# Optimization experiments

Measured on AMD Instinct MI355X. Metric: run time of the kernel, lower is better.

## Reference

```python
import jax, jax.numpy as jnp
import numpy as np
from functools import partial

EPS = 1e-5
TAU = 0.1

def bn(x, g, b, axes):
    m = jnp.mean(x, axis=axes, keepdims=True)
    v = jnp.var(x, axis=axes, keepdims=True)
    return (x - m) * jax.lax.rsqrt(v + EPS) * g + b

def conv(x, w, b):
    # x: NCHW, w: OIHW, stride 1, padding 1
    y = jax.lax.conv_general_dilated(x, w, (1, 1), ((1, 1), (1, 1)),
                                     dimension_numbers=('NCHW', 'OIHW', 'NCHW'))
    return y + b[None, :, None, None]

def maxpool2(x):
    return jax.lax.reduce_window(x, -jnp.inf, jax.lax.max, (1, 1, 2, 2), (1, 1, 2, 2), 'VALID')

def setup_inputs() -> dict:
    key = jax.random.key(0)
    ks = jax.random.split(key, 24)
    s = 0.02
    B = 4096
    d = {}
    d['input_data'] = jax.random.normal(ks[0], (B, 3, 32, 32), jnp.float32)
    d['conv1_w'] = jax.random.normal(ks[1], (32, 3, 3, 3), jnp.float32) * s
    d['conv1_b'] = jnp.zeros((32,), jnp.float32)
    d['bn1_g'] = jnp.ones((32,), jnp.float32); d['bn1_b'] = jnp.zeros((32,), jnp.float32)
    d['conv2_w'] = jax.random.normal(ks[2], (64, 32, 3, 3), jnp.float32) * s
    d['conv2_b'] = jnp.zeros((64,), jnp.float32)
    d['bn2_g'] = jnp.ones((64,), jnp.float32); d['bn2_b'] = jnp.zeros((64,), jnp.float32)
    d['conv3_w'] = jax.random.normal(ks[3], (128, 64, 3, 3), jnp.float32) * s
    d['conv3_b'] = jnp.zeros((128,), jnp.float32)
    d['bn3_g'] = jnp.ones((128,), jnp.float32); d['bn3_b'] = jnp.zeros((128,), jnp.float32)
    d['pre_w'] = jax.random.normal(ks[4], (1024, 8192), jnp.float32) * s
    d['pre_b'] = jnp.zeros((1024,), jnp.float32)
    d['bnp_g'] = jnp.ones((1024,), jnp.float32); d['bnp_b'] = jnp.zeros((1024,), jnp.float32)
    d['disc_w'] = jax.random.normal(ks[5], (384, 1024), jnp.float32) * s
    d['disc_b'] = jnp.zeros((384,), jnp.float32)
    d['bnd_g'] = jnp.ones((384,), jnp.float32); d['bnd_b'] = jnp.zeros((384,), jnp.float32)
    d['dfc_w'] = jax.random.normal(ks[6], (2, 384), jnp.float32) * s
    d['dfc_b'] = jnp.zeros((2,), jnp.float32)
    d['sw_w'] = jax.random.normal(ks[7], (2, 384), jnp.float32) * s
    d['sw_b'] = jnp.zeros((2,), jnp.float32)
    # partitioned classifier: P=2, Linear(1024 -> 192) + ReLU + Linear(192 -> 10)
    d['p1_w'] = jax.random.normal(ks[8], (2, 192, 1024), jnp.float32) * s
    d['p1_b'] = jnp.zeros((2, 192), jnp.float32)
    d['p2_w'] = jax.random.normal(ks[9], (2, 10, 192), jnp.float32) * s
    d['p2_b'] = jnp.zeros((2, 10), jnp.float32)
    return d

def reference(input_data, conv1_w, conv1_b, bn1_g, bn1_b, conv2_w, conv2_b, bn2_g, bn2_b,
              conv3_w, conv3_b, bn3_g, bn3_b, pre_w, pre_b, bnp_g, bnp_b,
              disc_w, disc_b, bnd_g, bnd_b, dfc_w, dfc_b, sw_w, sw_b,
              p1_w, p1_b, p2_w, p2_b):
    B = input_data.shape[0]
    # feature extractor
    x = jax.nn.relu(bn(conv(input_data, conv1_w, conv1_b), bn1_g[None, :, None, None], bn1_b[None, :, None, None], (0, 2, 3)))
    x = maxpool2(x)
    x = jax.nn.relu(bn(conv(x, conv2_w, conv2_b), bn2_g[None, :, None, None], bn2_b[None, :, None, None], (0, 2, 3)))
    x = maxpool2(x)
    x = jax.nn.relu(bn(conv(x, conv3_w, conv3_b), bn3_g[None, :, None, None], bn3_b[None, :, None, None], (0, 2, 3)))
    feat = x.reshape(B, -1)  # [B, 8192]
    feat = jax.nn.relu(bn(feat @ pre_w.T + pre_b, bnp_g[None, :], bnp_b[None, :], (0,)))  # [B, 1024]
    # discriminator branch
    dpen = jax.nn.relu(bn(feat @ disc_w.T + disc_b, bnd_g[None, :], bnd_b[None, :], (0,)))  # [B, 384]
    domain_output = dpen @ dfc_w.T + dfc_b  # [B, 2]
    sw_logits = dpen @ sw_w.T + sw_b  # [B, P]
    # gumbel-softmax (soft) + multinomial sample of partition
    key = jax.random.key(42)
    k1, k2 = jax.random.split(key)
    u = jax.random.uniform(k1, sw_logits.shape, jnp.float32, 1e-10, 1.0)
    gumbel = -jnp.log(-jnp.log(u))
    y = jax.nn.softmax((sw_logits + gumbel) / TAU, axis=-1)  # [B, P]
    partition_idx = jax.random.categorical(k2, jnp.log(y + 1e-20), axis=-1)  # [B]
    # per-partition expert MLP computed densely (P=2), then gather chosen partition
    h = jax.nn.relu(jnp.einsum('bi,poi->pbo', feat, p1_w) + p1_b[:, None, :])  # [P, B, 192]
    logits = jnp.einsum('pbo,pco->pbc', h, p2_w) + p2_b[:, None, :]  # [P, B, 10]
    sel = logits[partition_idx, jnp.arange(B)]  # [B, 10]
    # original multiplies single-element stack by full gumbel vector and sums -> scale by sum(y)=1
    class_output_partitioned = sel * jnp.sum(y, axis=1, keepdims=True)
    return (class_output_partitioned, domain_output, partition_idx)
```

## Files before the change

kernel.cpp:

```cpp
#include <hip/hip_runtime.h>
#include <cstdint>
#include <cstddef>

typedef __attribute__((ext_vector_type(8))) short short8;
typedef __attribute__((ext_vector_type(4))) float f32x4;

__host__ __device__ inline void threefry2x32(uint32_t k0, uint32_t k1,
                                             uint32_t x0, uint32_t x1,
                                             uint32_t& o0, uint32_t& o1) {
  uint32_t ks2 = k0 ^ k1 ^ 0x1BD11BDAu;
  uint32_t v0 = x0 + k0, v1 = x1 + k1;
#define TF_R(r) { v0 += v1; v1 = (v1 << (r)) | (v1 >> (32 - (r))); v1 ^= v0; }
  TF_R(13) TF_R(15) TF_R(26) TF_R(6)
  v0 += k1; v1 += ks2 + 1u;
  TF_R(17) TF_R(29) TF_R(16) TF_R(24)
  v0 += ks2; v1 += k0 + 2u;
  TF_R(13) TF_R(15) TF_R(26) TF_R(6)
  v0 += k0; v1 += k1 + 3u;
  TF_R(17) TF_R(29) TF_R(16) TF_R(24)
  v0 += k1; v1 += ks2 + 4u;
  TF_R(13) TF_R(15) TF_R(26) TF_R(6)
  v0 += ks2; v1 += k0 + 5u;
#undef TF_R
  o0 = v0; o1 = v1;
}

__device__ __forceinline__ uint32_t tf_bits32(uint32_t k0, uint32_t k1, uint32_t j) {
  uint32_t o0, o1;
  threefry2x32(k0, k1, 0u, j, o0, o1);
  return o0 ^ o1;
}

__device__ __forceinline__ float u01_from_bits(uint32_t bits) {
  return __uint_as_float((bits >> 9) | 0x3f800000u) - 1.0f;
}

__device__ __forceinline__ float waveSum(float v) {
#pragma unroll
  for (int off = 32; off > 0; off >>= 1) v += __shfl_down(v, off, 64);
  return v;
}

__global__ __launch_bounds__(256) void conv1_fused_kernel(
    const float* __restrict__ in, const float* __restrict__ w,
    float* __restrict__ outraw, float* __restrict__ partials) {
  __shared__ float ins[3 * 34 * 34];
  __shared__ float red[4][64];
  const int b = blockIdx.x, t = threadIdx.x;
  for (int i = t; i < 3 * 34 * 34; i += 256) {
    int ci = i / 1156, r = i % 1156, iy = r / 34, ix = r % 34;
    int y = iy - 1, x = ix - 1;
    float v = 0.f;
    if ((unsigned)y < 32u && (unsigned)x < 32u)
      v = in[(((size_t)b * 3 + ci) * 32 + y) * 32 + x];
    ins[i] = v;
  }
  __syncthreads();
  const int py = t >> 4, px = t & 15, wv = t >> 6, ln = t & 63;
  float win[3][4][4];
#pragma unroll
  for (int ci = 0; ci < 3; ci++)
#pragma unroll
    for (int r = 0; r < 4; r++)
#pragma unroll
      for (int c = 0; c < 4; c++)
        win[ci][r][c] = ins[ci * 1156 + (2 * py + r) * 34 + (2 * px + c)];
#pragma unroll 1
  for (int co = 0; co < 32; co++) {
    float acc00 = 0.f, acc01 = 0.f, acc10 = 0.f, acc11 = 0.f;
#pragma unroll
    for (int ci = 0; ci < 3; ci++) {
      const float* wp = w + (co * 3 + ci) * 9;
#pragma unroll
      for (int dy = 0; dy < 3; dy++)
#pragma unroll
        for (int dx = 0; dx < 3; dx++) {
          float wvv = wp[dy * 3 + dx];
          acc00 += win[ci][dy][dx] * wvv;
          acc01 += win[ci][dy][dx + 1] * wvv;
          acc10 += win[ci][dy + 1][dx] * wvv;
          acc11 += win[ci][dy + 1][dx + 1] * wvv;
        }
    }
    float sm = acc00 + acc01 + acc10 + acc11;
    float sq = acc00 * acc00 + acc01 * acc01 + acc10 * acc10 + acc11 * acc11;
    float s = waveSum(sm), q = waveSum(sq);
    if (ln == 0) { red[wv][2 * co] = s; red[wv][2 * co + 1] = q; }
    float m = fmaxf(fmaxf(acc00, acc01), fmaxf(acc10, acc11));
    outraw[(((size_t)b * 32 + co) * 16 + py) * 16 + px] = m;
  }
  __syncthreads();
  for (int i = t; i < 64; i += 256)
    partials[(size_t)b * 64 + i] = red[0][i] + red[1][i] + red[2][i] + red[3][i];
}

__device__ __forceinline__ uint32_t pack_bf16q(float x) {
  uint32_t u = __float_as_uint(x);
  uint32_t hi = u & 0xffff0000u;
  float r = x - __uint_as_float(hi);
  uint32_t lo = __float_as_uint(r) >> 16;
  return hi | lo;
}

__device__ __forceinline__ uint4 pk4bn(float4 v, float sc, float sh) {
  uint4 o;
  o.x = pack_bf16q(fmaxf(v.x * sc + sh, 0.f));
  o.y = pack_bf16q(fmaxf(v.y * sc + sh, 0.f));
  o.z = pack_bf16q(fmaxf(v.z * sc + sh, 0.f));
  o.w = pack_bf16q(fmaxf(v.w * sc + sh, 0.f));
  return o;
}

__global__ void cvt_bf16q_kernel(const float* X, uint32_t* Y, int n4) {
  int i = blockIdx.x * blockDim.x + threadIdx.x;
  if (i >= n4) return;
  float4 x = ((const float4*)X)[i];
  uint4 o;
  o.x = pack_bf16q(x.x); o.y = pack_bf16q(x.y);
  o.z = pack_bf16q(x.z); o.w = pack_bf16q(x.w);
  ((uint4*)Y)[i] = o;
}

__global__ void prep_w2_kernel(const float* __restrict__ w, short* __restrict__ wh,
                               short* __restrict__ wl) {
  int idx = blockIdx.x * 256 + threadIdx.x;
  if (idx >= 64 * 32 * 9) return;
  int tp = idx % 9, rem = idx / 9;
  int ci = rem % 32, co = rem / 32;
  uint32_t pq = pack_bf16q(w[idx]);
  size_t o = ((size_t)tp * 64 + co) * 32 + ci;
  wh[o] = (short)(pq >> 16);
  wl[o] = (short)(pq & 0xffffu);
}

__global__ void prep_w3_kernel(const float* __restrict__ w, short* __restrict__ wh,
                               short* __restrict__ wl) {
  int idx = blockIdx.x * 256 + threadIdx.x;
  if (idx >= 128 * 64 * 9) return;
  int tp = idx % 9, rem = idx / 9;
  int ci = rem % 64, co = rem / 64;
  uint32_t pq = pack_bf16q(w[idx]);
  size_t o = ((size_t)tp * 128 + co) * 64 + ci;
  wh[o] = (short)(pq >> 16);
  wl[o] = (short)(pq & 0xffffu);
}

#define STORE2(ARR_H, ARR_L, ROW, KB, SW, U, V)                                 \
  {                                                                             \
    uint32_t h0 = (U.x >> 16) | (U.y & 0xffff0000u);                            \
    uint32_t h1 = (U.z >> 16) | (U.w & 0xffff0000u);                            \
    uint32_t h2 = (V.x >> 16) | (V.y & 0xffff0000u);                            \
    uint32_t h3 = (V.z >> 16) | (V.w & 0xffff0000u);                            \
    uint32_t l0 = (U.x & 0xffffu) | (U.y << 16);                                \
    uint32_t l1 = (U.z & 0xffffu) | (U.w << 16);                                \
    uint32_t l2 = (V.x & 0xffffu) | (V.y << 16);                                \
    uint32_t l3 = (V.z & 0xffffu) | (V.w << 16);                                \
    int idx = (ROW) * 32 + ((KB) ^ (SW));                                       \
    *(uint4*)&ARR_H[idx] = make_uint4(h0, h1, h2, h3);                          \
    *(uint4*)&ARR_L[idx] = make_uint4(l0, l1, l2, l3);                          \
  }

__global__ __launch_bounds__(256) void conv2_mfma_kernel(
    const float* __restrict__ in, const float* __restrict__ scale1,
    const float* __restrict__ shift1, const short* __restrict__ wh,
    const short* __restrict__ wl, float* __restrict__ outpool,
    float* __restrict__ partials) {
  __shared__ short Xh[324 * 32], Xl[324 * 32];
  __shared__ float red[4][128];
  const int b = blockIdx.x, t = threadIdx.x;
  for (int i = t; i < 324 * 16; i += 256) {
    int row = i >> 4;
    int py = row / 18, pxx = row % 18;
    if (py == 0 || py == 17 || pxx == 0 || pxx == 17) {
      ((uint32_t*)Xh)[i] = 0u;
      ((uint32_t*)Xl)[i] = 0u;
    }
  }
  for (int i = t; i < 4096; i += 256) {
    int p = i >> 8, px = i & 255;
    int y = px >> 4, x = px & 15;
    float va = in[((size_t)b * 32 + 2 * p) * 256 + px];
    float vb = in[((size_t)b * 32 + 2 * p + 1) * 256 + px];
    va = fmaxf(va * scale1[2 * p] + shift1[2 * p], 0.f);
    vb = fmaxf(vb * scale1[2 * p + 1] + shift1[2 * p + 1], 0.f);
    uint32_t ua = pack_bf16q(va), ub = pack_bf16q(vb);
    uint32_t h = (ua >> 16) | (ub & 0xffff0000u);
    uint32_t l = (ua & 0xffffu) | (ub << 16);
    int row = (y + 1) * 18 + (x + 1);
    int ci2 = (2 * p) ^ ((row & 3) << 3);
    ((uint32_t*)Xh)[(row * 32 + ci2) >> 1] = h;
    ((uint32_t*)Xl)[(row * 32 + ci2) >> 1] = l;
  }
  __syncthreads();
  const int w = t >> 6, l = t & 63;
  const int lr = l & 15, lg = l >> 4;
  f32x4 acc[4][4];
#pragma unroll
  for (int i = 0; i < 4; i++)
#pragma unroll
    for (int j = 0; j < 4; j++) acc[i][j] = (f32x4){0.f, 0.f, 0.f, 0.f};
#pragma unroll 1
  for (int tap = 0; tap < 9; tap++) {
    const int dy = tap / 3, dx = tap % 3;
    short8 awh[4], awl[4];
#pragma unroll
    for (int i = 0; i < 4; i++) {
      size_t off = ((size_t)tap * 64 + i * 16 + lr) * 32 + lg * 8;
      awh[i] = *(const short8*)(wh + off);
      awl[i] = *(const short8*)(wl + off);
    }
    short8 bxh[4], bxl[4];
#pragma unroll
    for (int j = 0; j < 4; j++) {
      int y = w * 4 + j, x = lr;
      int row = (y + dy) * 18 + (x + dx);
      int ci = (lg * 8) ^ ((row & 3) << 3);
      bxh[j] = *(const short8*)&Xh[row * 32 + ci];
      bxl[j] = *(const short8*)&Xl[row * 32 + ci];
    }
#pragma unroll
    for (int i = 0; i < 4; i++)
#pragma unroll
      for (int j = 0; j < 4; j++) {
        acc[i][j] = __builtin_amdgcn_mfma_f32_16x16x32_bf16(awh[i], bxh[j], acc[i][j], 0, 0, 0);
        acc[i][j] = __builtin_amdgcn_mfma_f32_16x16x32_bf16(awh[i], bxl[j], acc[i][j], 0, 0, 0);
        acc[i][j] = __builtin_amdgcn_mfma_f32_16x16x32_bf16(awl[i], bxh[j], acc[i][j], 0, 0, 0);
      }
  }
#pragma unroll
  for (int i = 0; i < 4; i++)
#pragma unroll
    for (int r = 0; r < 4; r++) {
      int co = i * 16 + lg * 4 + r;
      float v0 = acc[i][0][r], v1 = acc[i][1][r], v2 = acc[i][2][r], v3 = acc[i][3][r];
      float s = v0 + v1 + v2 + v3;
      float q = v0 * v0 + v1 * v1 + v2 * v2 + v3 * v3;
#pragma unroll
      for (int off = 1; off <= 8; off <<= 1) {
        s += __shfl_xor(s, off, 64);
        q += __shfl_xor(q, off, 64);
      }
      if (lr == 0) { red[w][2 * co] = s; red[w][2 * co + 1] = q; }
      float h0 = fmaxf(v0, __shfl_xor(v0, 1, 64));
      float h1 = fmaxf(v1, __shfl_xor(v1, 1, 64));
      float h2 = fmaxf(v2, __shfl_xor(v2, 1, 64));
      float h3 = fmaxf(v3, __shfl_xor(v3, 1, 64));
      float pm0 = fmaxf(h0, h1);
      float pm1 = fmaxf(h2, h3);
      if ((lr & 1) == 0) {
        size_t base = ((size_t)b * 64 + co) * 64 + (w * 2) * 8 + (lr >> 1);
        outpool[base] = pm0;
        outpool[base + 8] = pm1;
      }
    }
  __syncthreads();
  for (int i = t; i < 128; i += 256)
    partials[(size_t)b * 128 + i] = red[0][i] + red[1][i] + red[2][i] + red[3][i];
}

__global__ __launch_bounds__(256) void conv3_mfma_kernel(
    const float* __restrict__ in, const float* __restrict__ scale2,
    const float* __restrict__ shift2, const short* __restrict__ wh,
    const short* __restrict__ wl, float* __restrict__ outraw,
    float* __restrict__ partials) {
  __shared__ short Xh[100 * 64], Xl[100 * 64];
  __shared__ float red[256];
  const int b = blockIdx.x, t = threadIdx.x;
  for (int i = t; i < 100 * 32; i += 256) {
    int row = i >> 5;
    int py = row / 10, pxx = row % 10;
    if (py == 0 || py == 9 || pxx == 0 || pxx == 9) {
      ((uint32_t*)Xh)[i] = 0u;
      ((uint32_t*)Xl)[i] = 0u;
    }
  }
  for (int i = t; i < 2048; i += 256) {
    int p = i >> 6, px = i & 63;
    int y = px >> 3, x = px & 7;
    float va = in[((size_t)b * 64 + 2 * p) * 64 + px];
    float vb = in[((size_t)b * 64 + 2 * p + 1) * 64 + px];
    va = fmaxf(va * scale2[2 * p] + shift2[2 * p], 0.f);
    vb = fmaxf(vb * scale2[2 * p + 1] + shift2[2 * p + 1], 0.f);
    uint32_t ua = pack_bf16q(va), ub = pack_bf16q(vb);
    uint32_t h = (ua >> 16) | (ub & 0xffff0000u);
    uint32_t l = (ua & 0xffffu) | (ub << 16);
    int row = (y + 1) * 10 + (x + 1);
    int ci2 = (2 * p) ^ ((row & 7) << 3);
    ((uint32_t*)Xh)[(row * 64 + ci2) >> 1] = h;
    ((uint32_t*)Xl)[(row * 64 + ci2) >> 1] = l;
  }
  __syncthreads();
  const int w = t >> 6, l = t & 63;
  const int lr = l & 15, lg = l >> 4;
  const int co_base = w * 32;
  f32x4 acc[2][4];
#pragma unroll
  for (int i = 0; i < 2; i++)
#pragma unroll
    for (int j = 0; j < 4; j++) acc[i][j] = (f32x4){0.f, 0.f, 0.f, 0.f};
#pragma unroll 1
  for (int tap = 0; tap < 9; tap++) {
    const int dy = tap / 3, dx = tap % 3;
#pragma unroll
    for (int sl = 0; sl < 2; sl++) {
      short8 awh[2], awl[2];
#pragma unroll
      for (int i = 0; i < 2; i++) {
        size_t off = ((size_t)tap * 128 + co_base + i * 16 + lr) * 64 + sl * 32 + lg * 8;
        awh[i] = *(const short8*)(wh + off);
        awl[i] = *(const short8*)(wl + off);
      }
      short8 bxh[4], bxl[4];
#pragma unroll
      for (int j = 0; j < 4; j++) {
        int px = j * 16 + lr;
        int row = ((px >> 3) + dy) * 10 + (px & 7) + dx;
        int ci = (sl * 32 + lg * 8) ^ ((row & 7) << 3);
        bxh[j] = *(const short8*)&Xh[row * 64 + ci];
        bxl[j] = *(const short8*)&Xl[row * 64 + ci];
      }
#pragma unroll
      for (int i = 0; i < 2; i++)
#pragma unroll
        for (int j = 0; j < 4; j++) {
          acc[i][j] = __builtin_amdgcn_mfma_f32_16x16x32_bf16(awh[i], bxh[j], acc[i][j], 0, 0, 0);
          acc[i][j] = __builtin_amdgcn_mfma_f32_16x16x32_bf16(awh[i], bxl[j], acc[i][j], 0, 0, 0);
          acc[i][j] = __builtin_amdgcn_mfma_f32_16x16x32_bf16(awl[i], bxh[j], acc[i][j], 0, 0, 0);
        }
    }
  }
#pragma unroll
  for (int i = 0; i < 2; i++)
#pragma unroll
    for (int r = 0; r < 4; r++) {
      int co = co_base + i * 16 + lg * 4 + r;
      float s = 0.f, q = 0.f;
#pragma unroll
      for (int j = 0; j < 4; j++) {
        float v = acc[i][j][r];
        outraw[((size_t)b * 128 + co) * 64 + j * 16 + lr] = v;
        s += v; q += v * v;
      }
#pragma unroll
      for (int off = 1; off <= 8; off <<= 1) {
        s += __shfl_xor(s, off, 64);
        q += __shfl_xor(q, off, 64);
      }
      if (lr == 0) { red[2 * co] = s; red[2 * co + 1] = q; }
    }
  __syncthreads();
  for (int i = t; i < 256; i += 256) partials[(size_t)b * 256 + i] = red[i];
}

__global__ __launch_bounds__(256) void reduce_partials_kernel(
    const float* __restrict__ partials, int nblk, int Q, double* __restrict__ sums) {
  int q = blockIdx.x;
  double acc = 0.0;
  for (int i = threadIdx.x; i < nblk; i += 256) acc += (double)partials[(size_t)i * Q + q];
  __shared__ double red[256];
  red[threadIdx.x] = acc;
  __syncthreads();
  for (int s = 128; s > 0; s >>= 1) {
    if (threadIdx.x < s) red[threadIdx.x] += red[threadIdx.x + s];
    __syncthreads();
  }
  if (threadIdx.x == 0) sums[q] = red[0];
}

__global__ __launch_bounds__(1024) void col_stats_kernel(
    const float* __restrict__ X, const float* __restrict__ Y,
    int R, int C, int nch, double* __restrict__ sums) {
  int c0 = blockIdx.x * 64, chunk = blockIdx.y;
  int cl = threadIdx.x & 63, rg = threadIdx.x >> 6;
  int rows = R / nch, rbeg = chunk * rows, rend = rbeg + rows;
  double s = 0.0, sq = 0.0;
  for (int r = rbeg + rg; r < rend; r += 16) {
    size_t idx = (size_t)r * C + c0 + cl;
    float v = X[idx];
    if (Y) v += Y[idx];
    s += v; sq += (double)v * (double)v;
  }
  __shared__ double red[16][64][2];
  red[rg][cl][0] = s; red[rg][cl][1] = sq;
  __syncthreads();
  if (rg == 0) {
    for (int i = 1; i < 16; i++) { s += red[i][cl][0]; sq += red[i][cl][1]; }
    sums[(size_t)chunk * 2 * C + 2 * (c0 + cl)] = s;
    sums[(size_t)chunk * 2 * C + 2 * (c0 + cl) + 1] = sq;
  }
}

__global__ void bn_finalize_kernel(const double* __restrict__ sums, int nch, int cst2,
                                   const float* __restrict__ g, const float* __restrict__ b,
                                   float* __restrict__ scale, float* __restrict__ shift,
                                   int C, double invN) {
  int c = blockIdx.x * blockDim.x + threadIdx.x;
  if (c >= C) return;
  double s = 0.0, sq = 0.0;
  for (int ch = 0; ch < nch; ch++) {
    s += sums[(size_t)ch * cst2 + 2 * c];
    sq += sums[(size_t)ch * cst2 + 2 * c + 1];
  }
  double m = s * invN;
  double v = sq * invN - m * m;
  double sc = (double)g[c] / sqrt(v + 1e-5);
  scale[c] = (float)sc;
  shift[c] = (float)((double)b[c] - m * sc);
}

__global__ void bn_relu_pack_cols4_kernel(float* __restrict__ X,
                                          const float* __restrict__ Y,
                                          const float* __restrict__ scale,
                                          const float* __restrict__ shift,
                                          int n4, int C4) {
  int i = blockIdx.x * blockDim.x + threadIdx.x;
  if (i >= n4) return;
  int c4 = i % C4;
  float4 v = ((float4*)X)[i];
  if (Y) {
    float4 y = ((const float4*)Y)[i];
    v.x += y.x; v.y += y.y; v.z += y.z; v.w += y.w;
  }
  float4 sc = ((const float4*)scale)[c4];
  float4 sh = ((const float4*)shift)[c4];
  uint4 o;
  o.x = pack_bf16q(fmaxf(v.x * sc.x + sh.x, 0.f));
  o.y = pack_bf16q(fmaxf(v.y * sc.y + sh.y, 0.f));
  o.z = pack_bf16q(fmaxf(v.z * sc.z + sh.z, 0.f));
  o.w = pack_bf16q(fmaxf(v.w * sc.w + sh.w, 0.f));
  ((uint4*)X)[i] = o;
}

__global__ void bn_relu_cols4_kernel(float* __restrict__ X, const float* __restrict__ scale,
                                     const float* __restrict__ shift, int n4, int C4) {
  int i = blockIdx.x * blockDim.x + threadIdx.x;
  if (i >= n4) return;
  int c4 = i % C4;
  float4 v = ((float4*)X)[i];
  float4 sc = ((const float4*)scale)[c4];
  float4 sh = ((const float4*)shift)[c4];
  v.x = fmaxf(v.x * sc.x + sh.x, 0.f);
  v.y = fmaxf(v.y * sc.y + sh.y, 0.f);
  v.z = fmaxf(v.z * sc.z + sh.z, 0.f);
  v.w = fmaxf(v.w * sc.w + sh.w, 0.f);
  ((float4*)X)[i] = v;
}

__device__ __forceinline__ int swz16(int row) {
  return ((row & 3) ^ ((row >> 2) & 3)) << 3;
}

template <int BIASRELU>
__global__ __launch_bounds__(256) void gemm_bf16q_kernel(
    const uint32_t* __restrict__ A, const uint32_t* __restrict__ B,
    const float* __restrict__ bias, float* __restrict__ C, int M, int N, int K) {
  __shared__ short Ah[128 * 32], Al[128 * 32], Bh[64 * 32], Bl[64 * 32];
  const int t = threadIdx.x;
  const int nTN = N >> 6;
  const int mPer = (M >> 7) >> 3;
  const int bid = blockIdx.x;
  const int xcd = bid & 7, qq = bid >> 3;
  const int m0 = (xcd * mPer + qq / nTN) << 7;
  const int n0 = (qq % nTN) << 6;
  const int w = t >> 6, l = t & 63;
  const int wrow = (w >> 1) << 6, wcol = (w & 1) << 5;
  const int lr = l & 15, lg = l >> 4;
  const int ar = t >> 1, akh = (t & 1) << 4;
  const int br = t >> 2, bkh = (t & 3) << 3;
  const int asw = swz16(ar), bsw = swz16(br);
  const uint32_t* Ap = A + (size_t)(m0 + ar) * K + akh;
  const uint32_t* Bp = B + (size_t)(n0 + br) * K + bkh;
  f32x4 acc[4][2];
#pragma unroll
  for (int i = 0; i < 4; i++)
#pragma unroll
    for (int j = 0; j < 2; j++) acc[i][j] = (f32x4){0.f, 0.f, 0.f, 0.f};
  uint4 ra0 = *(const uint4*)(Ap + 0), ra1 = *(const uint4*)(Ap + 4);
  uint4 ra2 = *(const uint4*)(Ap + 8), ra3 = *(const uint4*)(Ap + 12);
  uint4 rb0 = *(const uint4*)(Bp + 0), rb1 = *(const uint4*)(Bp + 4);
  const int NS = K >> 5;
  for (int s = 0; s < NS; s++) {
    __syncthreads();
    STORE2(Ah, Al, ar, akh + 0, asw, ra0, ra1)
    STORE2(Ah, Al, ar, akh + 8, asw, ra2, ra3)
    STORE2(Bh, Bl, br, bkh, bsw, rb0, rb1)
    __syncthreads();
    if (s + 1 < NS) {
      int ko = (s + 1) << 5;
      ra0 = *(const uint4*)(Ap + ko); ra1 = *(const uint4*)(Ap + ko + 4);
      ra2 = *(const uint4*)(Ap + ko + 8); ra3 = *(const uint4*)(Ap + ko + 12);
      rb0 = *(const uint4*)(Bp + ko); rb1 = *(const uint4*)(Bp + ko + 4);
    }
    short8 ahf[4], alf[4], bhf[2], blf[2];
#pragma unroll
    for (int i = 0; i < 4; i++) {
      int R = wrow + i * 16 + lr;
      int kk = (lg << 3) ^ swz16(R);
      ahf[i] = *(const short8*)&Ah[R * 32 + kk];
      alf[i] = *(const short8*)&Al[R * 32 + kk];
    }
#pragma unroll
    for (int j = 0; j < 2; j++) {
      int Cc = wcol + j * 16 + lr;
      int kk = (lg << 3) ^ swz16(Cc);
      bhf[j] = *(const short8*)&Bh[Cc * 32 + kk];
      blf[j] = *(const short8*)&Bl[Cc * 32 + kk];
    }
#pragma unroll
    for (int i = 0; i < 4; i++)
#pragma unroll
      for (int j = 0; j < 2; j++) {
        acc[i][j] = __builtin_amdgcn_mfma_f32_16x16x32_bf16(ahf[i], bhf[j], acc[i][j], 0, 0, 0);
        acc[i][j] = __builtin_amdgcn_mfma_f32_16x16x32_bf16(ahf[i], blf[j], acc[i][j], 0, 0, 0);
        acc[i][j] = __builtin_amdgcn_mfma_f32_16x16x32_bf16(alf[i], bhf[j], acc[i][j], 0, 0, 0);
      }
  }
#pragma unroll
  for (int i = 0; i < 4; i++)
#pragma unroll
    for (int j = 0; j < 2; j++) {
      int n = n0 + wcol + j * 16 + lr;
#pragma unroll
      for (int r = 0; r < 4; r++) {
        int m = m0 + wrow + i * 16 + lg * 4 + r;
        float v = acc[i][j][r];
        if (BIASRELU) v = fmaxf(v + bias[n], 0.f);
        C[(size_t)m * N + n] = v;
      }
    }
}

__global__ __launch_bounds__(256, 2) void gemm_bf16q_big_kernel(
    const float* __restrict__ A, const uint32_t* __restrict__ B,
    const float* __restrict__ scale, const float* __restrict__ shift,
    float* __restrict__ C0, float* __restrict__ C1, int M, int N, int K) {
  __shared__ short Ah[128 * 32], Al[128 * 32], Bh[128 * 32], Bl[128 * 32];
  const int t = threadIdx.x;
  const int nTN = N >> 7;
  const int tiles = (M >> 7) * nTN;
  const int mPer = (M >> 7) >> 3;
  const int split = blockIdx.x / tiles;
  const int bid = blockIdx.x % tiles;
  const int xcd = bid & 7, qq = bid >> 3;
  const int m0 = (xcd * mPer + qq / nTN) << 7;
  const int n0 = (qq % nTN) << 7;
  const int Kh = K >> 1;
  const int kbeg = split * Kh;
  float* Cout = split ? C1 : C0;
  const int w = t >> 6, l = t & 63;
  const int wrow = (w & 1) << 6, wcol = (w >> 1) << 6;
  const int lr = l & 15, lg = l >> 4;
  const int ar = t >> 1, akh = (t & 1) << 4;
  const int asw = swz16(ar);
  const float* Ap = A + (size_t)(m0 + ar) * K + kbeg + akh;
  const uint32_t* Bp = B + (size_t)(n0 + ar) * K + kbeg + akh;
  f32x4 acc[4][4];
#pragma unroll
  for (int i = 0; i < 4; i++)
#pragma unroll
    for (int j = 0; j < 4; j++) acc[i][j] = (f32x4){0.f, 0.f, 0.f, 0.f};
  float4 fa0 = *(const float4*)(Ap + 0), fa1 = *(const float4*)(Ap + 4);
  float4 fa2 = *(const float4*)(Ap + 8), fa3 = *(const float4*)(Ap + 12);
  uint4 rb0 = *(const uint4*)(Bp + 0), rb1 = *(const uint4*)(Bp + 4);
  uint4 rb2 = *(const uint4*)(Bp + 8), rb3 = *(const uint4*)(Bp + 12);
  const int NS = Kh >> 5;
  for (int s = 0; s < NS; s++) {
    int ch = (kbeg + akh + (s << 5)) >> 6;
    float sc = scale[ch], sh = shift[ch];
    uint4 ua0 = pk4bn(fa0, sc, sh), ua1 = pk4bn(fa1, sc, sh);
    uint4 ua2 = pk4bn(fa2, sc, sh), ua3 = pk4bn(fa3, sc, sh);
    __syncthreads();
    STORE2(Ah, Al, ar, akh + 0, asw, ua0, ua1)
    STORE2(Ah, Al, ar, akh + 8, asw, ua2, ua3)
    STORE2(Bh, Bl, ar, akh + 0, asw, rb0, rb1)
    STORE2(Bh, Bl, ar, akh + 8, asw, rb2, rb3)
    __syncthreads();
    if (s + 1 < NS) {
      int ko = (s + 1) << 5;
      fa0 = *(const float4*)(Ap + ko); fa1 = *(const float4*)(Ap + ko + 4);
      fa2 = *(const float4*)(Ap + ko + 8); fa3 = *(const float4*)(Ap + ko + 12);
      rb0 = *(const uint4*)(Bp + ko); rb1 = *(const uint4*)(Bp + ko + 4);
      rb2 = *(const uint4*)(Bp + ko + 8); rb3 = *(const uint4*)(Bp + ko + 12);
    }
    short8 ahf[4], alf[4], bhf[4], blf[4];
#pragma unroll
    for (int i = 0; i < 4; i++) {
      int R = wrow + i * 16 + lr;
      int kk = (lg << 3) ^ swz16(R);
      ahf[i] = *(const short8*)&Ah[R * 32 + kk];
      alf[i] = *(const short8*)&Al[R * 32 + kk];
    }
#pragma unroll
    for (int j = 0; j < 4; j++) {
      int Cc = wcol + j * 16 + lr;
      int kk = (lg << 3) ^ swz16(Cc);
      bhf[j] = *(const short8*)&Bh[Cc * 32 + kk];
      blf[j] = *(const short8*)&Bl[Cc * 32 + kk];
    }
#pragma unroll
    for (int i = 0; i < 4; i++)
#pragma unroll
      for (int j = 0; j < 4; j++) {
        acc[i][j] = __builtin_amdgcn_mfma_f32_16x16x32_bf16(ahf[i], bhf[j], acc[i][j], 0, 0, 0);
        acc[i][j] = __builtin_amdgcn_mfma_f32_16x16x32_bf16(ahf[i], blf[j], acc[i][j], 0, 0, 0);
        acc[i][j] = __builtin_amdgcn_mfma_f32_16x16x32_bf16(alf[i], bhf[j], acc[i][j], 0, 0, 0);
      }
  }
#pragma unroll
  for (int i = 0; i < 4; i++)
#pragma unroll
    for (int j = 0; j < 4; j++) {
      int n = n0 + wcol + j * 16 + lr;
#pragma unroll
      for (int r = 0; r < 4; r++) {
        int m = m0 + wrow + i * 16 + lg * 4 + r;
        Cout[(size_t)m * N + n] = acc[i][j][r];
      }
    }
}

__global__ __launch_bounds__(256) void heads_kernel(
    const float* __restrict__ dpen, const float* __restrict__ dfc_w,
    const float* __restrict__ dfc_b, const float* __restrict__ sw_w,
    const float* __restrict__ sw_b, float* __restrict__ out_dom,
    float* __restrict__ swbuf) {
  int wv = threadIdx.x >> 6, ln = threadIdx.x & 63;
  int b = blockIdx.x * 4 + wv;
  const float* row = dpen + (size_t)b * 384;
  double a0 = 0.0, a1 = 0.0, a2 = 0.0, a3 = 0.0;
  for (int k = ln; k < 384; k += 64) {
    double rv = (double)row[k];
    a0 += rv * (double)dfc_w[k];
    a1 += rv * (double)dfc_w[384 + k];
    a2 += rv * (double)sw_w[k];
    a3 += rv * (double)sw_w[384 + k];
  }
#pragma unroll
  for (int off = 32; off > 0; off >>= 1) {
    a0 += __shfl_down(a0, off, 64);
    a1 += __shfl_down(a1, off, 64);
    a2 += __shfl_down(a2, off, 64);
    a3 += __shfl_down(a3, off, 64);
  }
  if (ln == 0) {
    out_dom[b * 2 + 0] = (float)(a0 + (double)dfc_b[0]);
    out_dom[b * 2 + 1] = (float)(a1 + (double)dfc_b[1]);
    swbuf[b * 2 + 0] = (float)(a2 + (double)sw_b[0]);
    swbuf[b * 2 + 1] = (float)(a3 + (double)sw_b[1]);
  }
}

__global__ __launch_bounds__(256) void partition_kernel(
    const float* __restrict__ swbuf, float* __restrict__ out_pid,
    int* __restrict__ pidxI, float* __restrict__ ysum,
    uint32_t k1a, uint32_t k1b, uint32_t k2a, uint32_t k2b) {
  int b = blockIdx.x * 256 + threadIdx.x;
  if (b >= 4096) return;
  uint32_t j0 = (uint32_t)(2 * b), j1 = (uint32_t)(2 * b + 1);
  float f0 = u01_from_bits(tf_bits32(k1a, k1b, j0));
  float f1 = u01_from_bits(tf_bits32(k1a, k1b, j1));
  const float MINV = 1e-10f;
  float u0 = fmaxf(MINV, f0 * (1.0f - MINV) + MINV);
  float u1 = fmaxf(MINV, f1 * (1.0f - MINV) + MINV);
  double g0 = -log(-log((double)u0));
  double g1 = -log(-log((double)u1));
  double s0 = (double)swbuf[2 * b], s1 = (double)swbuf[2 * b + 1];
  double x0 = (s0 + g0) / 0.1;
  double x1 = (s1 + g1) / 0.1;
  double mx = fmax(x0, x1);
  double e0 = exp(x0 - mx), e1 = exp(x1 - mx);
  double es = e0 + e1;
  double y0 = e0 / es, y1 = e1 / es;
  float h0 = u01_from_bits(tf_bits32(k2a, k2b, j0));
  float h1 = u01_from_bits(tf_bits32(k2a, k2b, j1));
  const float TINY = 1.17549435e-38f;
  float v0 = fmaxf(TINY, h0 * (1.0f - TINY) + TINY);
  float v1 = fmaxf(TINY, h1 * (1.0f - TINY) + TINY);
  double gg0 = -log(-log((double)v0));
  double gg1 = -log(-log((double)v1));
  double l0 = log(y0 + 1e-20) + gg0;
  double l1 = log(y1 + 1e-20) + gg1;
  int p = (l1 > l0) ? 1 : 0;
  out_pid[b] = (float)p;
  pidxI[b] = p;
  ysum[b] = (float)(y0 + y1);
}

__global__ __launch_bounds__(256) void final_kernel(
    const float* __restrict__ h, const float* __restrict__ p2w,
    const float* __restrict__ p2b, const int* __restrict__ pidxI,
    const float* __restrict__ ysum, float* __restrict__ out0) {
  int t = blockIdx.x * 256 + threadIdx.x;
  if (t >= 40960) return;
  int b = t / 10, c = t % 10;
  int p = pidxI[b];
  const float* hr = h + (size_t)b * 384 + p * 192;
  const float* wr = p2w + ((size_t)p * 10 + c) * 192;
  float s = 0.f;
  for (int o = 0; o < 192; o++) s += hr[o] * wr[o];
  s += p2b[p * 10 + c];
  out0[t] = s * ysum[b];
}

extern "C" void kernel_launch(void* const* d_in, const int* in_sizes, int n_in,
                              void* d_out, int out_size, void* d_ws, size_t ws_size,
                              hipStream_t stream) {
  const float* input   = (const float*)d_in[0];
  const float* conv1_w = (const float*)d_in[1];
  const float* bn1_g   = (const float*)d_in[3];
  const float* bn1_b   = (const float*)d_in[4];
  const float* conv2_w = (const float*)d_in[5];
  const float* bn2_g   = (const float*)d_in[7];
  const float* bn2_b   = (const float*)d_in[8];
  const float* conv3_w = (const float*)d_in[9];
  const float* bn3_g   = (const float*)d_in[11];
  const float* bn3_b   = (const float*)d_in[12];
  const float* pre_w   = (const float*)d_in[13];
  const float* bnp_g   = (const float*)d_in[15];
  const float* bnp_b   = (const float*)d_in[16];
  const float* disc_w  = (const float*)d_in[17];
  const float* bnd_g   = (const float*)d_in[19];
  const float* bnd_b   = (const float*)d_in[20];
  const float* dfc_w   = (const float*)d_in[21];
  const float* dfc_b   = (const float*)d_in[22];
  const float* sw_w    = (const float*)d_in[23];
  const float* sw_b    = (const float*)d_in[24];
  const float* p1_w    = (const float*)d_in[25];
  const float* p1_b    = (const float*)d_in[26];
  const float* p2_w    = (const float*)d_in[27];
  const float* p2_b    = (const float*)d_in[28];

  float* W = (float*)d_ws;
  float* pool1  = W + 0;
  float* pool2  = W + 33554432;
  float* act3   = W + 0;
  uint32_t* Bcvt = (uint32_t*)(W + 33554432);
  uint32_t* discq = (uint32_t*)(W + 41943040);
  uint32_t* p1q   = (uint32_t*)(W + 42336256);
  float* csplit = W + 42729472;
  float* featp  = W + 50331648;
  uint32_t* featq = (uint32_t*)featp;
  short* wh3    = (short*)(W + 50331648);
  short* wl3    = (short*)(W + 50368512);
  short* wh2    = (short*)(W + 50405376);
  short* wl2    = (short*)(W + 50414592);
  float* dpen   = W + 54525952;
  float* hbuf   = W + 56098816;
  float* swbuf  = W + 57671680;
  float* ysum   = W + 57679872;
  int*   pidxI  = (int*)(W + 57683968);
  float* part   = W + 57688064;
  double* sums  = (double*)(W + 58736640);
  float* scale  = W + 58769408;
  float* shift  = W + 58770432;

  float* out_cls = (float*)d_out;
  float* out_dom = out_cls + 40960;
  float* out_pid = out_cls + 49152;

  uint32_t k1a, k1b, k2a, k2b;
  threefry2x32(0u, 42u, 0u, 0u, k1a, k1b);
  threefry2x32(0u, 42u, 0u, 1u, k2a, k2b);

  conv1_fused_kernel<<<dim3(4096), dim3(256), 0, stream>>>(input, conv1_w, pool1, part);
  reduce_partials_kernel<<<dim3(64), dim3(256), 0, stream>>>(part, 4096, 64, sums);
  bn_finalize_kernel<<<dim3(1), dim3(64), 0, stream>>>(sums, 1, 0, bn1_g, bn1_b, scale, shift, 32, 1.0 / (4096.0 * 1024.0));

  prep_w2_kernel<<<dim3(72), dim3(256), 0, stream>>>(conv2_w, wh2, wl2);
  conv2_mfma_kernel<<<dim3(4096), dim3(256), 0, stream>>>(pool1, scale, shift, wh2, wl2, pool2, part);
  reduce_partials_kernel<<<dim3(128), dim3(256), 0, stream>>>(part, 4096, 128, sums);
  bn_finalize_kernel<<<dim3(1), dim3(64), 0, stream>>>(sums, 1, 0, bn2_g, bn2_b, scale, shift, 64, 1.0 / (4096.0 * 256.0));

  prep_w3_kernel<<<dim3(288), dim3(256), 0, stream>>>(conv3_w, wh3, wl3);
  conv3_mfma_kernel<<<dim3(4096), dim3(256), 0, stream>>>(pool2, scale, shift, wh3, wl3, act3, part);
  reduce_partials_kernel<<<dim3(256), dim3(256), 0, stream>>>(part, 4096, 256, sums);
  bn_finalize_kernel<<<dim3(1), dim3(128), 0, stream>>>(sums, 1, 0, bn3_g, bn3_b, scale, shift, 128, 1.0 / (4096.0 * 64.0));

  cvt_bf16q_kernel<<<dim3(8192), dim3(256), 0, stream>>>(pre_w, Bcvt, 2097152);
  gemm_bf16q_big_kernel<<<dim3(512), dim3(256), 0, stream>>>(act3, Bcvt, scale, shift, featp, csplit, 4096, 1024, 8192);
  col_stats_kernel<<<dim3(16, 8), dim3(1024), 0, stream>>>(featp, csplit, 4096, 1024, 8, sums);
  bn_finalize_kernel<<<dim3(4), dim3(256), 0, stream>>>(sums, 8, 2048, bnp_g, bnp_b, scale, shift, 1024, 1.0 / 4096.0);
  bn_relu_pack_cols4_kernel<<<dim3(4096), dim3(256), 0, stream>>>(featp, csplit, scale, shift, 1048576, 256);

  cvt_bf16q_kernel<<<dim3(384), dim3(256), 0, stream>>>(disc_w, discq, 98304);
  cvt_bf16q_kernel<<<dim3(384), dim3(256), 0, stream>>>(p1_w, p1q, 98304);
  gemm_bf16q_kernel<0><<<dim3(192), dim3(256), 0, stream>>>(featq, discq, (const float*)nullptr, dpen, 4096, 384, 1024);
  col_stats_kernel<<<dim3(6, 8), dim3(1024), 0, stream>>>(dpen, (const float*)nullptr, 4096, 384, 8, sums);
  bn_finalize_kernel<<<dim3(2), dim3(256), 0, stream>>>(sums, 8, 768, bnd_g, bnd_b, scale, shift, 384, 1.0 / 4096.0);
  bn_relu_cols4_kernel<<<dim3(1536), dim3(256), 0, stream>>>(dpen, scale, shift, 393216, 96);

  heads_kernel<<<dim3(1024), dim3(256), 0, stream>>>(dpen, dfc_w, dfc_b, sw_w, sw_b, out_dom, swbuf);
  partition_kernel<<<dim3(16), dim3(256), 0, stream>>>(swbuf, out_pid, pidxI, ysum, k1a, k1b, k2a, k2b);

  gemm_bf16q_kernel<1><<<dim3(192), dim3(256), 0, stream>>>(featq, p1q, p1_b, hbuf, 4096, 384, 1024);
  final_kernel<<<dim3(160), dim3(256), 0, stream>>>(hbuf, p2_w, p2_b, pidxI, ysum, out_cls);
}
```

Measured before the change: 851.4 us.

## Double-buffer big GEMM LDS, merge two small GEMMs, fuse BN reduce+finalize

The large pre-layer GEMM now double-buffers its shared-memory tiles, so the next K-slice is converted and stored while MFMAs run on the current one. This cuts the syncs per step from two to one, at the cost of twice the LDS (64 KB), which may lower occupancy. The discriminator and partition-p1 GEMMs become one launch of 384 blocks that pick their B matrix by block index, which fills more of the GPU. The conv BN partial reduction and finalize kernels are merged into one kernel per layer, removing launches.

```diff
diff --git a/kernel.cpp b/kernel.cpp
--- a/kernel.cpp
+++ b/kernel.cpp
@@ -352,19 +352,30 @@
   for (int i = t; i < 256; i += 256) partials[(size_t)b * 256 + i] = red[i];
 }
 
-__global__ __launch_bounds__(256) void reduce_partials_kernel(
-    const float* __restrict__ partials, int nblk, int Q, double* __restrict__ sums) {
-  int q = blockIdx.x;
-  double acc = 0.0;
-  for (int i = threadIdx.x; i < nblk; i += 256) acc += (double)partials[(size_t)i * Q + q];
-  __shared__ double red[256];
-  red[threadIdx.x] = acc;
+__global__ __launch_bounds__(256) void reduce_finalize_kernel(
+    const float* __restrict__ partials, int nblk, int Q,
+    const float* __restrict__ g, const float* __restrict__ b,
+    float* __restrict__ scale, float* __restrict__ shift, double invN) {
+  int c = blockIdx.x, t = threadIdx.x;
+  double s = 0.0, q = 0.0;
+  for (int i = t; i < nblk; i += 256) {
+    s += (double)partials[(size_t)i * Q + 2 * c];
+    q += (double)partials[(size_t)i * Q + 2 * c + 1];
+  }
+  __shared__ double rs[256], rq[256];
+  rs[t] = s; rq[t] = q;
   __syncthreads();
-  for (int s = 128; s > 0; s >>= 1) {
-    if (threadIdx.x < s) red[threadIdx.x] += red[threadIdx.x + s];
+  for (int st = 128; st > 0; st >>= 1) {
+    if (t < st) { rs[t] += rs[t + st]; rq[t] += rq[t + st]; }
     __syncthreads();
   }
-  if (threadIdx.x == 0) sums[q] = red[0];
+  if (t == 0) {
+    double m = rs[0] * invN;
+    double v = rq[0] * invN - m * m;
+    double sc = (double)g[c] / sqrt(v + 1e-5);
+    scale[c] = (float)sc;
+    shift[c] = (float)((double)b[c] - m * sc);
+  }
 }
 
 __global__ __launch_bounds__(1024) void col_stats_kernel(
@@ -450,15 +461,19 @@
   return ((row & 3) ^ ((row >> 2) & 3)) << 3;
 }
 
-template <int BIASRELU>
-__global__ __launch_bounds__(256) void gemm_bf16q_kernel(
-    const uint32_t* __restrict__ A, const uint32_t* __restrict__ B,
-    const float* __restrict__ bias, float* __restrict__ C, int M, int N, int K) {
+__global__ __launch_bounds__(256) void gemm_bf16q_dual_kernel(
+    const uint32_t* __restrict__ A, const uint32_t* __restrict__ B0,
+    const uint32_t* __restrict__ B1, const float* __restrict__ bias1,
+    float* __restrict__ C0, float* __restrict__ C1, int M, int N, int K) {
   __shared__ short Ah[128 * 32], Al[128 * 32], Bh[64 * 32], Bl[64 * 32];
   const int t = threadIdx.x;
   const int nTN = N >> 6;
+  const int tiles = (M >> 7) * nTN;
+  const int half = (blockIdx.x >= tiles) ? 1 : 0;
+  const uint32_t* B = half ? B1 : B0;
+  float* C = half ? C1 : C0;
+  const int bid = blockIdx.x - half * tiles;
   const int mPer = (M >> 7) >> 3;
-  const int bid = blockIdx.x;
   const int xcd = bid & 7, qq = bid >> 3;
   const int m0 = (xcd * mPer + qq / nTN) << 7;
   const int n0 = (qq % nTN) << 6;
@@ -524,7 +539,7 @@
       for (int r = 0; r < 4; r++) {
         int m = m0 + wrow + i * 16 + lg * 4 + r;
         float v = acc[i][j][r];
-        if (BIASRELU) v = fmaxf(v + bias[n], 0.f);
+        if (half) v = fmaxf(v + bias1[n], 0.f);
         C[(size_t)m * N + n] = v;
       }
     }
@@ -534,7 +549,7 @@
     const float* __restrict__ A, const uint32_t* __restrict__ B,
     const float* __restrict__ scale, const float* __restrict__ shift,
     float* __restrict__ C0, float* __restrict__ C1, int M, int N, int K) {
-  __shared__ short Ah[128 * 32], Al[128 * 32], Bh[128 * 32], Bl[128 * 32];
+  __shared__ short Ah[2][128 * 32], Al[2][128 * 32], Bh[2][128 * 32], Bl[2][128 * 32];
   const int t = threadIdx.x;
   const int nTN = N >> 7;
   const int tiles = (M >> 7) * nTN;
@@ -559,43 +574,62 @@
   for (int i = 0; i < 4; i++)
 #pragma unroll
     for (int j = 0; j < 4; j++) acc[i][j] = (f32x4){0.f, 0.f, 0.f, 0.f};
+  const int NS = Kh >> 5;
   float4 fa0 = *(const float4*)(Ap + 0), fa1 = *(const float4*)(Ap + 4);
   float4 fa2 = *(const float4*)(Ap + 8), fa3 = *(const float4*)(Ap + 12);
   uint4 rb0 = *(const uint4*)(Bp + 0), rb1 = *(const uint4*)(Bp + 4);
   uint4 rb2 = *(const uint4*)(Bp + 8), rb3 = *(const uint4*)(Bp + 12);
-  const int NS = Kh >> 5;
-  for (int s = 0; s < NS; s++) {
-    int ch = (kbeg + akh + (s << 5)) >> 6;
+  {
+    int ch = (kbeg + akh) >> 6;
     float sc = scale[ch], sh = shift[ch];
     uint4 ua0 = pk4bn(fa0, sc, sh), ua1 = pk4bn(fa1, sc, sh);
     uint4 ua2 = pk4bn(fa2, sc, sh), ua3 = pk4bn(fa3, sc, sh);
-    __syncthreads();
-    STORE2(Ah, Al, ar, akh + 0, asw, ua0, ua1)
-    STORE2(Ah, Al, ar, akh + 8, asw, ua2, ua3)
-    STORE2(Bh, Bl, ar, akh + 0, asw, rb0, rb1)
-    STORE2(Bh, Bl, ar, akh + 8, asw, rb2, rb3)
-    __syncthreads();
-    if (s + 1 < NS) {
-      int ko = (s + 1) << 5;
-      fa0 = *(const float4*)(Ap + ko); fa1 = *(const float4*)(Ap + ko + 4);
-      fa2 = *(const float4*)(Ap + ko + 8); fa3 = *(const float4*)(Ap + ko + 12);
-      rb0 = *(const uint4*)(Bp + ko); rb1 = *(const uint4*)(Bp + ko + 4);
-      rb2 = *(const uint4*)(Bp + ko + 8); rb3 = *(const uint4*)(Bp + ko + 12);
-    }
+    STORE2(Ah[0], Al[0], ar, akh + 0, asw, ua0, ua1)
+    STORE2(Ah[0], Al[0], ar, akh + 8, asw, ua2, ua3)
+    STORE2(Bh[0], Bl[0], ar, akh + 0, asw, rb0, rb1)
+    STORE2(Bh[0], Bl[0], ar, akh + 8, asw, rb2, rb3)
+  }
+  if (NS > 1) {
+    fa0 = *(const float4*)(Ap + 32); fa1 = *(const float4*)(Ap + 36);
+    fa2 = *(const float4*)(Ap + 40); fa3 = *(const float4*)(Ap + 44);
+    rb0 = *(const uint4*)(Bp + 32); rb1 = *(const uint4*)(Bp + 36);
+    rb2 = *(const uint4*)(Bp + 40); rb3 = *(const uint4*)(Bp + 44);
+  }
+  __syncthreads();
+  int cur = 0;
+  for (int s = 0; s < NS; s++) {
     short8 ahf[4], alf[4], bhf[4], blf[4];
 #pragma unroll
     for (int i = 0; i < 4; i++) {
       int R = wrow + i * 16 + lr;
       int kk = (lg << 3) ^ swz16(R);
-      ahf[i] = *(const short8*)&Ah[R * 32 + kk];
-      alf[i] = *(const short8*)&Al[R * 32 + kk];
+      ahf[i] = *(const short8*)&Ah[cur][R * 32 + kk];
+      alf[i] = *(const short8*)&Al[cur][R * 32 + kk];
     }
 #pragma unroll
     for (int j = 0; j < 4; j++) {
       int Cc = wcol + j * 16 + lr;
       int kk = (lg << 3) ^ swz16(Cc);
-      bhf[j] = *(const short8*)&Bh[Cc * 32 + kk];
-      blf[j] = *(const short8*)&Bl[Cc * 32 + kk];
+      bhf[j] = *(const short8*)&Bh[cur][Cc * 32 + kk];
+      blf[j] = *(const short8*)&Bl[cur][Cc * 32 + kk];
+    }
+    if (s + 1 < NS) {
+      int nxt = cur ^ 1;
+      int ch = (kbeg + akh + ((s + 1) << 5)) >> 6;
+      float sc = scale[ch], sh = shift[ch];
+      uint4 ua0 = pk4bn(fa0, sc, sh), ua1 = pk4bn(fa1, sc, sh);
+      uint4 ua2 = pk4bn(fa2, sc, sh), ua3 = pk4bn(fa3, sc, sh);
+      STORE2(Ah[nxt], Al[nxt], ar, akh + 0, asw, ua0, ua1)
+      STORE2(Ah[nxt], Al[nxt], ar, akh + 8, asw, ua2, ua3)
+      STORE2(Bh[nxt], Bl[nxt], ar, akh + 0, asw, rb0, rb1)
+      STORE2(Bh[nxt], Bl[nxt], ar, akh + 8, asw, rb2, rb3)
+      if (s + 2 < NS) {
+        int ko = (s + 2) << 5;
+        fa0 = *(const float4*)(Ap + ko); fa1 = *(const float4*)(Ap + ko + 4);
+        fa2 = *(const float4*)(Ap + ko + 8); fa3 = *(const float4*)(Ap + ko + 12);
+        rb0 = *(const uint4*)(Bp + ko); rb1 = *(const uint4*)(Bp + ko + 4);
+        rb2 = *(const uint4*)(Bp + ko + 8); rb3 = *(const uint4*)(Bp + ko + 12);
+      }
     }
 #pragma unroll
     for (int i = 0; i < 4; i++)
@@ -605,6 +639,8 @@
         acc[i][j] = __builtin_amdgcn_mfma_f32_16x16x32_bf16(ahf[i], blf[j], acc[i][j], 0, 0, 0);
         acc[i][j] = __builtin_amdgcn_mfma_f32_16x16x32_bf16(alf[i], bhf[j], acc[i][j], 0, 0, 0);
       }
+    __syncthreads();
+    cur ^= 1;
   }
 #pragma unroll
   for (int i = 0; i < 4; i++)
@@ -763,18 +799,15 @@
   threefry2x32(0u, 42u, 0u, 1u, k2a, k2b);
 
   conv1_fused_kernel<<<dim3(4096), dim3(256), 0, stream>>>(input, conv1_w, pool1, part);
-  reduce_partials_kernel<<<dim3(64), dim3(256), 0, stream>>>(part, 4096, 64, sums);
-  bn_finalize_kernel<<<dim3(1), dim3(64), 0, stream>>>(sums, 1, 0, bn1_g, bn1_b, scale, shift, 32, 1.0 / (4096.0 * 1024.0));
+  reduce_finalize_kernel<<<dim3(32), dim3(256), 0, stream>>>(part, 4096, 64, bn1_g, bn1_b, scale, shift, 1.0 / (4096.0 * 1024.0));
 
   prep_w2_kernel<<<dim3(72), dim3(256), 0, stream>>>(conv2_w, wh2, wl2);
   conv2_mfma_kernel<<<dim3(4096), dim3(256), 0, stream>>>(pool1, scale, shift, wh2, wl2, pool2, part);
-  reduce_partials_kernel<<<dim3(128), dim3(256), 0, stream>>>(part, 4096, 128, sums);
-  bn_finalize_kernel<<<dim3(1), dim3(64), 0, stream>>>(sums, 1, 0, bn2_g, bn2_b, scale, shift, 64, 1.0 / (4096.0 * 256.0));
+  reduce_finalize_kernel<<<dim3(64), dim3(256), 0, stream>>>(part, 4096, 128, bn2_g, bn2_b, scale, shift, 1.0 / (4096.0 * 256.0));
 
   prep_w3_kernel<<<dim3(288), dim3(256), 0, stream>>>(conv3_w, wh3, wl3);
   conv3_mfma_kernel<<<dim3(4096), dim3(256), 0, stream>>>(pool2, scale, shift, wh3, wl3, act3, part);
-  reduce_partials_kernel<<<dim3(256), dim3(256), 0, stream>>>(part, 4096, 256, sums);
-  bn_finalize_kernel<<<dim3(1), dim3(128), 0, stream>>>(sums, 1, 0, bn3_g, bn3_b, scale, shift, 128, 1.0 / (4096.0 * 64.0));
+  reduce_finalize_kernel<<<dim3(128), dim3(256), 0, stream>>>(part, 4096, 256, bn3_g, bn3_b, scale, shift, 1.0 / (4096.0 * 64.0));
 
   cvt_bf16q_kernel<<<dim3(8192), dim3(256), 0, stream>>>(pre_w, Bcvt, 2097152);
   gemm_bf16q_big_kernel<<<dim3(512), dim3(256), 0, stream>>>(act3, Bcvt, scale, shift, featp, csplit, 4096, 1024, 8192);
@@ -784,7 +817,7 @@
 
   cvt_bf16q_kernel<<<dim3(384), dim3(256), 0, stream>>>(disc_w, discq, 98304);
   cvt_bf16q_kernel<<<dim3(384), dim3(256), 0, stream>>>(p1_w, p1q, 98304);
-  gemm_bf16q_kernel<0><<<dim3(192), dim3(256), 0, stream>>>(featq, discq, (const float*)nullptr, dpen, 4096, 384, 1024);
+  gemm_bf16q_dual_kernel<<<dim3(384), dim3(256), 0, stream>>>(featq, discq, p1q, p1_b, dpen, hbuf, 4096, 384, 1024);
   col_stats_kernel<<<dim3(6, 8), dim3(1024), 0, stream>>>(dpen, (const float*)nullptr, 4096, 384, 8, sums);
   bn_finalize_kernel<<<dim3(2), dim3(256), 0, stream>>>(sums, 8, 768, bnd_g, bnd_b, scale, shift, 384, 1.0 / 4096.0);
   bn_relu_cols4_kernel<<<dim3(1536), dim3(256), 0, stream>>>(dpen, scale, shift, 393216, 96);
@@ -792,6 +825,5 @@
   heads_kernel<<<dim3(1024), dim3(256), 0, stream>>>(dpen, dfc_w, dfc_b, sw_w, sw_b, out_dom, swbuf);
   partition_kernel<<<dim3(16), dim3(256), 0, stream>>>(swbuf, out_pid, pidxI, ysum, k1a, k1b, k2a, k2b);
 
-  gemm_bf16q_kernel<1><<<dim3(192), dim3(256), 0, stream>>>(featq, p1q, p1_b, hbuf, 4096, 384, 1024);
   final_kernel<<<dim3(160), dim3(256), 0, stream>>>(hbuf, p2_w, p2_b, pidxI, ysum, out_cls);
 }
```

Result: faster. 826.9 us, median of 2 (-2.9%).
